# Kernel tuning notes

Hardware: AMD Instinct MI355X
Metric: run time of the kernel (lower is better)

## Reference

```python
import jax, jax.numpy as jnp
import numpy as np

B, C_IN, C_OUT, N, K, GROUPS = 4, 192, 192, 16384, 16, 4


def setup_inputs() -> dict:
    key = jax.random.key(0)
    k1, k2, k3, k4 = jax.random.split(key, 4)
    x = jax.random.normal(k1, (B, C_IN, N, 1), dtype=jnp.float32)
    edge_index = jax.random.randint(k2, (2, B, N, K), 0, N, dtype=jnp.int64)
    # Grouped 1x1 conv params (kaiming-normal-like init, zero bias)
    fan_in = C_IN // GROUPS
    weight = jax.random.normal(k3, (C_OUT, fan_in), dtype=jnp.float32) * np.sqrt(2.0 / fan_in)
    bias = jnp.zeros((C_OUT,), dtype=jnp.float32)
    eps = jnp.zeros((1,), dtype=jnp.float32)
    return {"x": x, "edge_index": edge_index, "weight": weight, "bias": bias, "eps": eps}


def reference(x, edge_index, weight, bias, eps):
    # x: (B, C, N, 1); edge_index: (2, B, N, K); weight: (C_OUT, C_IN//G); bias: (C_OUT,)
    idx = edge_index[0]  # (B, N, K)
    x_sq = x[:, :, :, 0]  # (B, C, N)
    # gather neighbor features per batch: (B, C, N, K)
    gather = jax.vmap(lambda xb, ib: xb[:, ib])(x_sq, idx)
    x_j = jnp.sum(gather, axis=-1)  # (B, C, N)  sum-aggregate
    h = (1.0 + eps[0]) * x_sq + x_j  # (B, C, N)
    # grouped 1x1 conv, groups=4
    g_in, g_out = C_IN // GROUPS, C_OUT // GROUPS
    hg = h.reshape(B, GROUPS, g_in, N)
    wg = weight.reshape(GROUPS, g_out, g_in)
    out = jnp.einsum('bgin,goi->bgon', hg, wg).reshape(B, C_OUT, N)
    out = out + bias[None, :, None]
    out = jax.nn.relu(out)
    return out[:, :, :, None]  # (B, C_OUT, N, 1)
```

## Files before the change

### kernel.cpp

```cpp
#include <hip/hip_runtime.h>
#include <hip/hip_fp16.h>

constexpr int B    = 4;
constexpr int CIN  = 192;
constexpr int COUT = 192;
constexpr int NN   = 16384;
constexpr int KK   = 16;
constexpr int NG   = 4;
constexpr int GIN  = 48;
constexpr int GOUT = 48;
constexpr int NT   = 64;
constexpr int TPB  = 192;
constexpr int IST  = 20;
constexpr int HST  = 56;
constexpr int WROW = 48;

constexpr float QMAX = 6.0f;
constexpr float QS   = QMAX / 127.0f;
constexpr float QSI  = 127.0f / QMAX;

typedef _Float16 v2h __attribute__((ext_vector_type(2)));
typedef float    v4f __attribute__((ext_vector_type(4)));

#if defined(__has_builtin)
#if __has_builtin(__builtin_amdgcn_fdot2)
#define FDOT2(a, b, c) __builtin_amdgcn_fdot2((a), (b), (c), false)
#endif
#endif
#ifndef FDOT2
__device__ __forceinline__ float FDOT2(v2h a, v2h b, float c) {
    return (float)a[0] * (float)b[0] + (float)a[1] * (float)b[1] + c;
}
#endif

__device__ __forceinline__ void store_nt4(float* p, float4 v) {
    v4f vv = {v.x, v.y, v.z, v.w};
    __builtin_nontemporal_store(vv, (v4f*)p);
}

__global__ __launch_bounds__(256) void transpose_q(const float* __restrict__ x,
                                                   unsigned char* __restrict__ xq) {
    __shared__ float tile[32][33];
    const int b  = blockIdx.z;
    const int n0 = blockIdx.x * 32;
    const int c0 = blockIdx.y * 32;
    const int tx = threadIdx.x;
    const int ty = threadIdx.y;
    const float* xb = x + (size_t)b * CIN * NN;
    unsigned char* xqb = xq + (size_t)b * NN * CIN;
#pragma unroll
    for (int i = 0; i < 32; i += 8)
        tile[ty + i][tx] = xb[(size_t)(c0 + ty + i) * NN + (n0 + tx)];
    __syncthreads();
#pragma unroll
    for (int i = 0; i < 32; i += 8) {
        const int c = c0 + tx, n = n0 + ty + i;
        float q = rintf(tile[tx][ty + i] * QSI) + 128.0f;
        q = fminf(fmaxf(q, 0.0f), 255.0f);
        xqb[((size_t)(c / GIN) * NN + n) * GIN + (c % GIN)] = (unsigned char)q;
    }
}

__device__ __forceinline__ void gemm_group(const __half* __restrict__ hg,
                                           const __half* __restrict__ wg,
                                           const float* __restrict__ bg,
                                           float* __restrict__ ob,
                                           int g, int n0, int e2, int r2) {
    float acc[4][4];
#pragma unroll
    for (int m = 0; m < 4; ++m) {
        const float bi = bg[r2 + 12 * m];
#pragma unroll
        for (int nd = 0; nd < 4; ++nd) acc[m][nd] = bi;
    }
#pragma unroll
    for (int ci8 = 0; ci8 < 6; ++ci8) {
        uint4 hq[4];
#pragma unroll
        for (int nd = 0; nd < 4; ++nd)
            hq[nd] = *(const uint4*)(hg + (nd * 16 + e2) * HST + ci8 * 8);
#pragma unroll
        for (int m = 0; m < 4; ++m) {
            const uint4 wq = *(const uint4*)(wg + (r2 + 12 * m) * WROW + ci8 * 8);
            const v2h* wv = (const v2h*)&wq;
#pragma unroll
            for (int nd = 0; nd < 4; ++nd) {
                const v2h* hv = (const v2h*)&hq[nd];
                acc[m][nd] = FDOT2(wv[0], hv[0], acc[m][nd]);
                acc[m][nd] = FDOT2(wv[1], hv[1], acc[m][nd]);
                acc[m][nd] = FDOT2(wv[2], hv[2], acc[m][nd]);
                acc[m][nd] = FDOT2(wv[3], hv[3], acc[m][nd]);
            }
        }
    }
#pragma unroll
    for (int m = 0; m < 4; ++m) {
        const float4 v = make_float4(fmaxf(acc[m][0], 0.0f),
                                     fmaxf(acc[m][1], 0.0f),
                                     fmaxf(acc[m][2], 0.0f),
                                     fmaxf(acc[m][3], 0.0f));
        store_nt4(ob + (size_t)(g * GOUT + r2 + 12 * m) * NN + n0 + 4 * e2, v);
    }
}

__global__ __launch_bounds__(TPB, 3) void gin_fused(const unsigned char* __restrict__ xq,
                                                    const int*   __restrict__ idx,
                                                    const float* __restrict__ w,
                                                    const float* __restrict__ bias,
                                                    const float* __restrict__ eps,
                                                    float* __restrict__ out) {
    __shared__ __align__(16) __half h16[NT * HST];
    __shared__ __align__(16) __half w16[NG * GOUT * WROW];
    __shared__ __align__(16) int    idx_lds[NT * IST];
    __shared__ float b_lds[COUT];

    const int tid = threadIdx.x;
    const int blk = blockIdx.x;
    const int b   = blk & 3;
    const int n0  = (blk >> 2) * NT;

    const float e1   = 1.0f + eps[0];
    const float e1qs = e1 * QS;
    const float cc   = -(QS * 2048.0f) - e1qs * 128.0f;

    {
        const int* gi = idx + ((size_t)b * NN + n0) * KK;
        for (int t = tid; t < NT * KK; t += TPB)
            idx_lds[(t >> 4) * IST + (t & 15)] = gi[t];
        b_lds[tid] = bias[tid];
        const float2* wp2 = (const float2*)w;
        __half2* wh2 = (__half2*)w16;
#pragma unroll
        for (int t = 0; t < 24; ++t) {
            const int lin = t * TPB + tid;
            wh2[lin] = __float22half2_rn(wp2[lin]);
        }
    }

    const int e3 = tid % 3;
    const int i  = tid / 3;
    const int e2 = tid & 15;
    const int r2 = tid >> 4;

    const unsigned char* xb = xq + (size_t)b * NN * CIN;
    float*               ob = out + (size_t)b * COUT * NN;

    __syncthreads();

    for (int g = 0; g < NG; ++g) {
        {
            const uint4* xg = (const uint4*)(xb + (size_t)g * NN * GIN);
            const int4* ip = (const int4*)(idx_lds + i * IST);
            const int4 ja = ip[0], jb = ip[1], jc = ip[2], jd = ip[3];
            const int js[16] = {ja.x, ja.y, ja.z, ja.w, jb.x, jb.y, jb.z, jb.w,
                                jc.x, jc.y, jc.z, jc.w, jd.x, jd.y, jd.z, jd.w};
            const uint4 us = xg[(size_t)(n0 + i) * 3 + e3];
            unsigned int aL[4] = {0u, 0u, 0u, 0u};
            unsigned int aH[4] = {0u, 0u, 0u, 0u};
#pragma unroll
            for (int t = 0; t < 16; ++t) {
                const uint4 u = xg[(size_t)js[t] * 3 + e3];
#pragma unroll
                for (int k = 0; k < 4; ++k) {
                    const unsigned int uw = (&u.x)[k];
                    aL[k] += uw & 0x00FF00FFu;
                    aH[k] += (uw >> 8) & 0x00FF00FFu;
                }
            }
            union { __half2 h2[8]; uint4 q[2]; } pk;
#pragma unroll
            for (int k = 0; k < 4; ++k) {
                const unsigned int uw = (&us.x)[k];
                const float s0 = (float)(aL[k] & 0xFFFFu);
                const float s1 = (float)(aH[k] & 0xFFFFu);
                const float s2 = (float)(aL[k] >> 16);
                const float s3 = (float)(aH[k] >> 16);
                const float f0 = (float)(uw & 0xFFu);
                const float f1 = (float)((uw >> 8) & 0xFFu);
                const float f2 = (float)((uw >> 16) & 0xFFu);
                const float f3 = (float)(uw >> 24);
                const float h0 = fmaf(QS, s0, fmaf(e1qs, f0, cc));
                const float h1 = fmaf(QS, s1, fmaf(e1qs, f1, cc));
                const float h2 = fmaf(QS, s2, fmaf(e1qs, f2, cc));
                const float h3 = fmaf(QS, s3, fmaf(e1qs, f3, cc));
                pk.h2[2 * k]     = __float22half2_rn(make_float2(h0, h1));
                pk.h2[2 * k + 1] = __float22half2_rn(make_float2(h2, h3));
            }
            __half* hrow = h16 + (size_t)((i & 3) * 16 + (i >> 2)) * HST + e3 * 16;
            *(uint4*)hrow       = pk.q[0];
            *(uint4*)(hrow + 8) = pk.q[1];
        }
        __syncthreads();
        __builtin_amdgcn_sched_barrier(0);

        gemm_group(h16, w16 + g * GOUT * WROW, b_lds + g * GOUT,
                   ob, g, n0, e2, r2);
        __syncthreads();
    }
}

extern "C" void kernel_launch(void* const* d_in, const int* in_sizes, int n_in,
                              void* d_out, int out_size, void* d_ws, size_t ws_size,
                              hipStream_t stream) {
    const float* x      = (const float*)d_in[0];
    const int*   edge   = (const int*)  d_in[1];
    const float* weight = (const float*)d_in[2];
    const float* bias   = (const float*)d_in[3];
    const float* eps    = (const float*)d_in[4];
    float*       out    = (float*)d_out;
    unsigned char* xq   = (unsigned char*)d_ws;

    dim3 tblk(32, 8);
    dim3 tgrd(NN / 32, CIN / 32, B);
    transpose_q<<<tgrd, tblk, 0, stream>>>(x, xq);

    gin_fused<<<B * (NN / NT), TPB, 0, stream>>>(xq, edge, weight, bias, eps, out);
}
```

Baseline: 49.72 us.

## Double-buffer gathered features and stagger gather/GEMM order across waves

```diff
diff --git a/kernel.cpp b/kernel.cpp
--- a/kernel.cpp
+++ b/kernel.cpp
@@ -61,6 +61,52 @@
     }
 }
 
+__device__ __forceinline__ void gather_i8(const uint4* __restrict__ xg,
+                                          const int* __restrict__ idx_lds,
+                                          int n0, int i, int e3,
+                                          float e1qs, float cc,
+                                          __half* __restrict__ hb) {
+    const int4* ip = (const int4*)(idx_lds + i * IST);
+    const int4 ja = ip[0], jb = ip[1], jc = ip[2], jd = ip[3];
+    const int js[16] = {ja.x, ja.y, ja.z, ja.w, jb.x, jb.y, jb.z, jb.w,
+                        jc.x, jc.y, jc.z, jc.w, jd.x, jd.y, jd.z, jd.w};
+    const uint4 us = xg[(size_t)(n0 + i) * 3 + e3];
+    unsigned int aL[4] = {0u, 0u, 0u, 0u};
+    unsigned int aH[4] = {0u, 0u, 0u, 0u};
+#pragma unroll
+    for (int t = 0; t < 16; ++t) {
+        const uint4 u = xg[(size_t)js[t] * 3 + e3];
+#pragma unroll
+        for (int k = 0; k < 4; ++k) {
+            const unsigned int uw = (&u.x)[k];
+            aL[k] += uw & 0x00FF00FFu;
+            aH[k] += (uw >> 8) & 0x00FF00FFu;
+        }
+    }
+    union { __half2 h2[8]; uint4 q[2]; } pk;
+#pragma unroll
+    for (int k = 0; k < 4; ++k) {
+        const unsigned int uw = (&us.x)[k];
+        const float s0 = (float)(aL[k] & 0xFFFFu);
+        const float s1 = (float)(aH[k] & 0xFFFFu);
+        const float s2 = (float)(aL[k] >> 16);
+        const float s3 = (float)(aH[k] >> 16);
+        const float f0 = (float)(uw & 0xFFu);
+        const float f1 = (float)((uw >> 8) & 0xFFu);
+        const float f2 = (float)((uw >> 16) & 0xFFu);
+        const float f3 = (float)(uw >> 24);
+        const float h0 = fmaf(QS, s0, fmaf(e1qs, f0, cc));
+        const float h1 = fmaf(QS, s1, fmaf(e1qs, f1, cc));
+        const float h2 = fmaf(QS, s2, fmaf(e1qs, f2, cc));
+        const float h3 = fmaf(QS, s3, fmaf(e1qs, f3, cc));
+        pk.h2[2 * k]     = __float22half2_rn(make_float2(h0, h1));
+        pk.h2[2 * k + 1] = __float22half2_rn(make_float2(h2, h3));
+    }
+    __half* hrow = hb + (size_t)((i & 3) * 16 + (i >> 2)) * HST + e3 * 16;
+    *(uint4*)hrow       = pk.q[0];
+    *(uint4*)(hrow + 8) = pk.q[1];
+}
+
 __device__ __forceinline__ void gemm_group(const __half* __restrict__ hg,
                                            const __half* __restrict__ wg,
                                            const float* __restrict__ bg,
@@ -109,7 +155,7 @@
                                                     const float* __restrict__ bias,
                                                     const float* __restrict__ eps,
                                                     float* __restrict__ out) {
-    __shared__ __align__(16) __half h16[NT * HST];
+    __shared__ __align__(16) __half h16[2][NT * HST];
     __shared__ __align__(16) __half w16[NG * GOUT * WROW];
     __shared__ __align__(16) int    idx_lds[NT * IST];
     __shared__ float b_lds[COUT];
@@ -141,60 +187,33 @@
     const int i  = tid / 3;
     const int e2 = tid & 15;
     const int r2 = tid >> 4;
+    const bool gemm_lead = ((tid >> 6) & 1);
 
     const unsigned char* xb = xq + (size_t)b * NN * CIN;
     float*               ob = out + (size_t)b * COUT * NN;
 
     __syncthreads();
 
+    gather_i8((const uint4*)xb, idx_lds, n0, i, e3, e1qs, cc, h16[0]);
+    __syncthreads();
+
+#pragma unroll
     for (int g = 0; g < NG; ++g) {
-        {
-            const uint4* xg = (const uint4*)(xb + (size_t)g * NN * GIN);
-            const int4* ip = (const int4*)(idx_lds + i * IST);
-            const int4 ja = ip[0], jb = ip[1], jc = ip[2], jd = ip[3];
-            const int js[16] = {ja.x, ja.y, ja.z, ja.w, jb.x, jb.y, jb.z, jb.w,
-                                jc.x, jc.y, jc.z, jc.w, jd.x, jd.y, jd.z, jd.w};
-            const uint4 us = xg[(size_t)(n0 + i) * 3 + e3];
-            unsigned int aL[4] = {0u, 0u, 0u, 0u};
-            unsigned int aH[4] = {0u, 0u, 0u, 0u};
-#pragma unroll
-            for (int t = 0; t < 16; ++t) {
-                const uint4 u = xg[(size_t)js[t] * 3 + e3];
-#pragma unroll
-                for (int k = 0; k < 4; ++k) {
-                    const unsigned int uw = (&u.x)[k];
-                    aL[k] += uw & 0x00FF00FFu;
-                    aH[k] += (uw >> 8) & 0x00FF00FFu;
-                }
-            }
-            union { __half2 h2[8]; uint4 q[2]; } pk;
-#pragma unroll
-            for (int k = 0; k < 4; ++k) {
-                const unsigned int uw = (&us.x)[k];
-                const float s0 = (float)(aL[k] & 0xFFFFu);
-                const float s1 = (float)(aH[k] & 0xFFFFu);
-                const float s2 = (float)(aL[k] >> 16);
-                const float s3 = (float)(aH[k] >> 16);
-                const float f0 = (float)(uw & 0xFFu);
-                const float f1 = (float)((uw >> 8) & 0xFFu);
-                const float f2 = (float)((uw >> 16) & 0xFFu);
-                const float f3 = (float)(uw >> 24);
-                const float h0 = fmaf(QS, s0, fmaf(e1qs, f0, cc));
-                const float h1 = fmaf(QS, s1, fmaf(e1qs, f1, cc));
-                const float h2 = fmaf(QS, s2, fmaf(e1qs, f2, cc));
-                const float h3 = fmaf(QS, s3, fmaf(e1qs, f3, cc));
-                pk.h2[2 * k]     = __float22half2_rn(make_float2(h0, h1));
-                pk.h2[2 * k + 1] = __float22half2_rn(make_float2(h2, h3));
-            }
-            __half* hrow = h16 + (size_t)((i & 3) * 16 + (i >> 2)) * HST + e3 * 16;
-            *(uint4*)hrow       = pk.q[0];
-            *(uint4*)(hrow + 8) = pk.q[1];
-        }
-        __syncthreads();
-        __builtin_amdgcn_sched_barrier(0);
-
-        gemm_group(h16, w16 + g * GOUT * WROW, b_lds + g * GOUT,
-                   ob, g, n0, e2, r2);
+        const __half* hcur = h16[g & 1];
+        __half*       hnxt = h16[(g & 1) ^ 1];
+        const uint4*  xgn  = (const uint4*)(xb + (size_t)(g + 1) * NN * GIN);
+        const __half* wg   = w16 + g * GOUT * WROW;
+        const float*  bg   = b_lds + g * GOUT;
+
+        if (gemm_lead) {
+            gemm_group(hcur, wg, bg, ob, g, n0, e2, r2);
+            if (g < NG - 1)
+                gather_i8(xgn, idx_lds, n0, i, e3, e1qs, cc, hnxt);
+        } else {
+            if (g < NG - 1)
+                gather_i8(xgn, idx_lds, n0, i, e3, e1qs, cc, hnxt);
+            gemm_group(hcur, wg, bg, ob, g, n0, e2, r2);
+        }
         __syncthreads();
     }
 }
```

Measured after the change: 52.75 us. +6.1%, slower.
